# Optimization experiments

Hardware: AMD Instinct MI355X
Metric: run time of the kernel (lower is better)

Reference implementation:

```python
import jax, jax.numpy as jnp
import numpy as np

B, S, D = 2, 2048, 2048
H, HKV = 16, 4
HD = D // H  # 128
ROPE_BASE = 10000.0


def _rope(t, cos, sin):
    # t: [B, h, S, HD]; torch variant: x1 = even dims, x2 = odd dims,
    # output = concat([x1*cos - x2*sin, x1*sin + x2*cos], axis=-1)
    x1 = t[..., ::2]
    x2 = t[..., 1::2]
    return jnp.concatenate([x1 * cos - x2 * sin, x1 * sin + x2 * cos], axis=-1)


def setup_inputs() -> dict:
    key = jax.random.key(0)
    kx, kq, kk, kv, ko = jax.random.split(key, 5)
    x = jax.random.normal(kx, (B, S, D), dtype=jnp.float32)
    scale = 0.02
    Wq = jax.random.normal(kq, (D, H * HD), dtype=jnp.float32) * scale
    Wk = jax.random.normal(kk, (D, HKV * HD), dtype=jnp.float32) * scale
    Wv = jax.random.normal(kv, (D, HKV * HD), dtype=jnp.float32) * scale
    Wo = jax.random.normal(ko, (H * HD, D), dtype=jnp.float32) * scale
    mask = jnp.tril(jnp.ones((S, S), dtype=bool))  # causal
    return {"x": x, "Wq": Wq, "Wk": Wk, "Wv": Wv, "Wo": Wo, "mask": mask}


def reference(x, Wq, Wk, Wv, Wo, mask):
    b, s, d = x.shape
    # projections: [B,S,h,HD] -> [B,h,S,HD]
    q = (x @ Wq).reshape(b, s, H, HD).transpose(0, 2, 1, 3)
    k = (x @ Wk).reshape(b, s, HKV, HD).transpose(0, 2, 1, 3)
    v = (x @ Wv).reshape(b, s, HKV, HD).transpose(0, 2, 1, 3)

    # RoPE tables: [S, HD/2]
    theta = 1.0 / (ROPE_BASE ** (jnp.arange(0, HD, 2, dtype=jnp.float32) / HD))
    angles = jnp.arange(s, dtype=jnp.float32)[:, None] * theta
    cos, sin = jnp.cos(angles), jnp.sin(angles)

    q = _rope(q, cos, sin)
    k = _rope(k, cos, sin)

    # GQA: repeat_interleave kv heads along head dim
    rep = H // HKV
    k = jnp.repeat(k, rep, axis=1)
    v = jnp.repeat(v, rep, axis=1)

    scores = jnp.einsum("bhqd,bhkd->bhqk", q, k) / jnp.sqrt(jnp.float32(HD))
    scores = jnp.where(mask, scores, -jnp.inf)
    attn = jax.nn.softmax(scores, axis=-1)

    out = jnp.einsum("bhqk,bhkd->bqhd", attn, v).reshape(b, s, H * HD)
    return out @ Wo
```

## Files before the change

kernel.cpp:

```cpp
#include <hip/hip_runtime.h>

typedef __bf16 bf16;
typedef __bf16 bf16x8 __attribute__((ext_vector_type(8)));
typedef float f32x4 __attribute__((ext_vector_type(4)));
typedef short s16x4 __attribute__((ext_vector_type(4)));

#define B_ 2
#define S_ 2048
#define D_ 2048
#define H_ 16
#define HKV_ 4
#define HD_ 128
#define QKVW 3072
#define QKW 2560
#define SCALE 0.08838834764831845f
#define NEGINF -30000.0f

__device__ inline void gload16(const void* g, void* l) {
  __builtin_amdgcn_global_load_lds((const __attribute__((address_space(1))) unsigned int*)g,
                                   (__attribute__((address_space(3))) unsigned int*)l, 16, 0, 0);
}

__device__ inline unsigned short bfb(float v) {
  union { bf16 h; unsigned short u; } c;
  c.h = (bf16)v;
  return c.u;
}

__global__ void detect_dtype(const unsigned* __restrict__ xw, int* __restrict__ flag) {
  __shared__ int cnt;
  if (threadIdx.x == 0) cnt = 0;
  __syncthreads();
  unsigned w = xw[(size_t)threadIdx.x * 16384];
  unsigned low = w & 0xFFFFu;
  int e = (int)((low >> 7) & 0xFF);
  int vote = (low == 0u || (e >= 100 && e <= 140)) ? 1 : 0;
  atomicAdd(&cnt, vote);
  __syncthreads();
  if (threadIdx.x == 0) *flag = (cnt >= 128) ? 1 : 0;
}

__global__ __launch_bounds__(256) void transpose_qkvw(
    const void* __restrict__ Wq, const void* __restrict__ Wk, const void* __restrict__ Wv,
    bf16* __restrict__ wqkvT, const int* __restrict__ flag) {
  int z = blockIdx.z;
  const void* in = (z == 0) ? Wq : (z == 1) ? Wk : Wv;
  int cols = (z == 0) ? 2048 : 512;
  bf16* out = wqkvT + ((z == 0) ? 0 : (z == 1) ? 2048 * 2048 : 2560 * 2048);
  if (blockIdx.x * 32 >= cols) return;
  int fm = *flag;
  __shared__ float tile[32][33];
  int c0 = blockIdx.x * 32, r0 = blockIdx.y * 32;
  int tx = threadIdx.x, ty = threadIdx.y;
#pragma unroll
  for (int i = 0; i < 32; i += 8) {
    long idx = (long)(r0 + ty + i) * cols + c0 + tx;
    tile[ty + i][tx] = fm ? (float)((const bf16*)in)[idx] : ((const float*)in)[idx];
  }
  __syncthreads();
#pragma unroll
  for (int i = 0; i < 32; i += 8)
    out[(long)(c0 + ty + i) * 2048 + r0 + tx] = (bf16)tile[tx][ty + i];
}

__global__ __launch_bounds__(256) void transpose_cvt(
    const void* __restrict__ in, bf16* __restrict__ out,
    long in_stride, long out_stride, const int* __restrict__ flag) {
  __shared__ float tile[32][33];
  int fm = *flag;
  int c0 = blockIdx.x * 32, r0 = blockIdx.y * 32;
  int tx = threadIdx.x, ty = threadIdx.y;
#pragma unroll
  for (int i = 0; i < 32; i += 8) {
    long idx = (long)(r0 + ty + i) * in_stride + c0 + tx;
    tile[ty + i][tx] = fm ? (float)((const bf16*)in)[idx] : ((const float*)in)[idx];
  }
  __syncthreads();
#pragma unroll
  for (int i = 0; i < 32; i += 8)
    out[(long)(c0 + ty + i) * out_stride + r0 + tx] = (bf16)tile[tx][ty + i];
}

#define BM 128
#define BN 128
#define BK 32

__global__ __launch_bounds__(256) void gemm_bt(
    const void* __restrict__ A, const bf16* __restrict__ Bt, void* __restrict__ C,
    int M, int N, int K, int ldc, int ncmax,
    bf16* __restrict__ vt_out, int vcol0,
    const int* __restrict__ flag, int adyn, int cdyn) {
  alignas(16) __shared__ bf16 la[BM * BK];
  alignas(16) __shared__ bf16 lb[BN * BK];
  int fm = flag ? *flag : 1;
  bool af32 = adyn && !fm;
  bool cf32 = cdyn && !fm;
  int tid = threadIdx.x;
  int wave = tid >> 6, lane = tid & 63;
  int wr = wave >> 1, wc = wave & 1;
  int quad = lane >> 4, l16 = lane & 15;
  int m0 = blockIdx.y * BM, n0 = blockIdx.x * BN;

  f32x4 acc[4][4] = {};

  int sr = (wave << 4) + (lane >> 2);
  int sc = (lane & 3) << 3;
  const bf16* gb0 = Bt + (long)(n0 + sr) * K + sc;
  const bf16* gb1 = Bt + (long)(n0 + 64 + sr) * K + sc;
  bf16* lb0 = lb + (wave << 9);
  bf16* lb1 = lb + 2048 + (wave << 9);
  bf16* la0 = la + (wave << 9);
  bf16* la1 = la + 2048 + (wave << 9);
  const bf16* ga0 = nullptr; const bf16* ga1 = nullptr;
  const float* gaf = nullptr;
  int fr = tid >> 1, fh = (tid & 1) << 4;
  if (af32) gaf = (const float*)A + (long)(m0 + fr) * K + fh;
  else { ga0 = (const bf16*)A + (long)(m0 + sr) * K + sc;
         ga1 = (const bf16*)A + (long)(m0 + 64 + sr) * K + sc; }
  bf16* law = la + fr * BK + fh;

  for (int k0 = 0; k0 < K; k0 += BK) {
    __syncthreads();
    gload16(gb0 + k0, lb0);
    gload16(gb1 + k0, lb1);
    if (af32) {
      const float* fp = gaf + k0;
      alignas(16) bf16 t[16];
#pragma unroll
      for (int u = 0; u < 16; u += 4) {
        float4 f = *(const float4*)(fp + u);
        t[u] = (bf16)f.x; t[u + 1] = (bf16)f.y; t[u + 2] = (bf16)f.z; t[u + 3] = (bf16)f.w;
      }
      *(uint4*)law = *(uint4*)t;
      *(uint4*)(law + 8) = *(uint4*)(t + 8);
    } else {
      gload16(ga0 + k0, la0);
      gload16(ga1 + k0, la1);
    }
    __syncthreads();

    const bf16* pa = la + ((wr << 6) + l16) * BK + (quad << 3);
    const bf16* pb = lb + ((wc << 6) + l16) * BK + (quad << 3);
    bf16x8 af[4], bfr[4];
#pragma unroll
    for (int i = 0; i < 4; i++) af[i] = *(const bf16x8*)(pa + (i << 4) * BK);
#pragma unroll
    for (int j = 0; j < 4; j++) bfr[j] = *(const bf16x8*)(pb + (j << 4) * BK);
#pragma unroll
    for (int i = 0; i < 4; i++)
#pragma unroll
      for (int j = 0; j < 4; j++)
        acc[i][j] = __builtin_amdgcn_mfma_f32_16x16x32_bf16(af[i], bfr[j], acc[i][j], 0, 0, 0);
  }

  if (vt_out && n0 >= vcol0) {
#pragma unroll
    for (int i = 0; i < 4; i++)
#pragma unroll
      for (int j = 0; j < 4; j++) {
        int col = n0 + (wc << 6) + (j << 4) + l16;
        int hdg = col - vcol0;
        int row0 = m0 + (wr << 6) + (i << 4) + (quad << 2);
        int bb = row0 >> 11, s = row0 & 2047;
        ushort4 p;
        p.x = bfb(acc[i][j][0]); p.y = bfb(acc[i][j][1]);
        p.z = bfb(acc[i][j][2]); p.w = bfb(acc[i][j][3]);
        *(ushort4*)(vt_out + (((long)(bb * 512 + hdg)) << 11) + s) = p;
      }
  } else {
#pragma unroll
    for (int i = 0; i < 4; i++)
#pragma unroll
      for (int j = 0; j < 4; j++) {
        int col = n0 + (wc << 6) + (j << 4) + l16;
        if (col >= ncmax) continue;
#pragma unroll
        for (int r = 0; r < 4; r++) {
          long row = m0 + (wr << 6) + (i << 4) + (quad << 2) + r;
          float v = acc[i][j][r];
          if (cf32) ((float*)C)[row * ldc + col] = v;
          else      ((bf16*)C)[row * ldc + col] = (bf16)v;
        }
      }
  }
}

__global__ __launch_bounds__(256) void rope_scatter(
    const bf16* __restrict__ qkv, bf16* __restrict__ Q, bf16* __restrict__ Ko) {
  int row = blockIdx.x;
  int b = row >> 11, s = row & 2047;
  int tid = threadIdx.x;
  const bf16* src = qkv + (long)row * QKW;
#pragma unroll
  for (int it = 0; it < 4; ++it) {
    int p = tid + it * 256;
    int h = p >> 6, i = p & 63;
    float x1 = (float)src[h * 128 + 2 * i];
    float x2 = (float)src[h * 128 + 2 * i + 1];
    float theta = __expf(-0.14391156831212787f * (float)i);
    float sn, cs;
    sincosf((float)s * theta, &sn, &cs);
    long qb = ((long)(b * H_ + h) * S_ + s) * HD_;
    Q[qb + i]      = (bf16)((x1 * cs - x2 * sn) * SCALE);
    Q[qb + 64 + i] = (bf16)((x1 * sn + x2 * cs) * SCALE);
  }
  {
    int kh = tid >> 6, i = tid & 63;
    float x1 = (float)src[2048 + kh * 128 + 2 * i];
    float x2 = (float)src[2048 + kh * 128 + 2 * i + 1];
    float theta = __expf(-0.14391156831212787f * (float)i);
    float sn, cs;
    sincosf((float)s * theta, &sn, &cs);
    long kb = ((long)(b * HKV_ + kh) * S_ + s) * HD_;
    Ko[kb + i]      = (bf16)(x1 * cs - x2 * sn);
    Ko[kb + 64 + i] = (bf16)(x1 * sn + x2 * cs);
  }
}

#define KTILE 8192
#define VTILE 8192

__global__ __launch_bounds__(256) void attn_kernel(
    const bf16* __restrict__ Q, const bf16* __restrict__ K,
    const bf16* __restrict__ Vt, bf16* __restrict__ O) {
  alignas(16) __shared__ bf16 Ks[2 * KTILE];
  alignas(16) __shared__ bf16 Vs[2 * VTILE];
  int qt0 = blockIdx.x;
  int h = blockIdx.y, b = blockIdx.z;
  int kh = h >> 2;
  int tid = threadIdx.x, wave = tid >> 6, lane = tid & 63;
  int quad = lane >> 4, l16 = lane & 15;
  const bf16* Kg = K + ((long)(b * HKV_ + kh) * S_) * HD_;
  const bf16* Vg = Vt + ((long)(b * HKV_ + kh) * HD_) * S_;

  int kgo[4], vgo[4], klo[4], vlo[4];
#pragma unroll
  for (int u = 0; u < 4; u++) {
    int i = u * 4 + wave;
    int r = i * 4 + quad;
    int c = l16 ^ (r & 15);
    kgo[u] = r * HD_ + c * 8;
    klo[u] = i * 512;
    int v = i * 8 + (lane >> 3);
    int cv = (lane & 7) ^ (v & 7);
    vgo[u] = v * S_ + cv * 8;
    vlo[u] = i * 512;
  }

  for (int hf = 0; hf < 2; ++hf) {
    int qt = hf ? 31 - qt0 : qt0;
    int q0 = qt * 64;
    const bf16* Qg = Q + ((long)(b * H_ + h) * S_ + q0) * HD_;

    bf16x8 qb[4];
    {
      const bf16* qrow = Qg + (wave * 16 + l16) * HD_ + quad * 8;
#pragma unroll
      for (int kk = 0; kk < 4; kk++) qb[kk] = *(const bf16x8*)(qrow + kk * 32);
    }

    if (hf) __syncthreads();

#pragma unroll
    for (int u = 0; u < 4; u++) {
      gload16(Kg + kgo[u], Ks + klo[u]);
      gload16(Vg + vgo[u], Vs + vlo[u]);
    }

    f32x4 Of[8] = {};
    float m_run = NEGINF, l_run = 0.f;

    for (int kt = 0; kt <= qt; ++kt) {
      __syncthreads();
      int p = kt & 1;
      if (kt < qt) {
        const bf16* kn = Kg + (long)(kt + 1) * 8192;
        const bf16* vn = Vg + (long)(kt + 1) * 64;
        bf16* kd = Ks + (p ^ 1) * KTILE;
        bf16* vd = Vs + (p ^ 1) * VTILE;
#pragma unroll
        for (int u = 0; u < 4; u++) {
          gload16(kn + kgo[u], kd + klo[u]);
          gload16(vn + vgo[u], vd + vlo[u]);
        }
      }
      const bf16* kc = Ks + p * KTILE;
      const bf16* vc = Vs + p * VTILE;

      bool diag = (kt == qt);
      f32x4 sf[4];
      __builtin_amdgcn_s_setprio(1);
#pragma unroll
      for (int jb = 0; jb < 4; jb++) {
        if (diag && jb > wave) {
          sf[jb] = (f32x4){NEGINF, NEGINF, NEGINF, NEGINF};
        } else {
          f32x4 a = {};
          const bf16* kbase = kc + (jb * 16 + l16) * 128;
#pragma unroll
          for (int kk = 0; kk < 4; kk++) {
            bf16x8 kf = *(const bf16x8*)(kbase + (((kk * 4 + quad) ^ l16) * 8));
            a = __builtin_amdgcn_mfma_f32_16x16x32_bf16(kf, qb[kk], a, 0, 0, 0);
          }
          sf[jb] = a;
        }
      }
      __builtin_amdgcn_s_setprio(0);
      if (diag) {
#pragma unroll
        for (int jb = 0; jb < 4; jb++)
          if (jb == wave) {
#pragma unroll
            for (int r = 0; r < 4; r++)
              if (quad * 4 + r > l16) sf[jb][r] = NEGINF;
          }
      }

      float mx = NEGINF;
#pragma unroll
      for (int jb = 0; jb < 4; jb++)
#pragma unroll
        for (int r = 0; r < 4; r++) mx = fmaxf(mx, sf[jb][r]);
      mx = fmaxf(mx, __shfl_xor(mx, 16));
      mx = fmaxf(mx, __shfl_xor(mx, 32));
      if (__any(mx > m_run + 8.0f)) {
        float mnew = fmaxf(m_run, mx);
        float alpha = __expf(m_run - mnew);
        m_run = mnew;
        l_run *= alpha;
#pragma unroll
        for (int n = 0; n < 8; n++) Of[n] *= alpha;
      }

      float ls = 0.f;
      s16x4 pk[4];
#pragma unroll
      for (int jb = 0; jb < 4; jb++) {
        float p0 = __expf(sf[jb][0] - m_run);
        float p1 = __expf(sf[jb][1] - m_run);
        float p2 = __expf(sf[jb][2] - m_run);
        float p3 = __expf(sf[jb][3] - m_run);
        ls += (p0 + p1) + (p2 + p3);
        s16x4 t;
        t.x = (short)bfb(p0); t.y = (short)bfb(p1);
        t.z = (short)bfb(p2); t.w = (short)bfb(p3);
        pk[jb] = t;
      }
      l_run += ls;

      __builtin_amdgcn_s_setprio(1);
#pragma unroll
      for (int jb = 0; jb < 4; jb++) {
        if (diag && jb > wave) continue;
#pragma unroll
        for (int n = 0; n < 8; n++) {
          int v = n * 16 + l16;
          const bf16* va_p = vc + v * 64 + (((jb * 2 + (quad >> 1)) ^ (l16 & 7)) * 8) + (quad & 1) * 4;
          s16x4 va = *(const s16x4*)va_p;
          Of[n] = __builtin_amdgcn_mfma_f32_16x16x16bf16_1k(va, pk[jb], Of[n], 0, 0, 0);
        }
      }
      __builtin_amdgcn_s_setprio(0);
    }

    l_run += __shfl_xor(l_run, 16);
    l_run += __shfl_xor(l_run, 32);
    float inv = 1.0f / fmaxf(l_run, 1e-30f);
    bf16* Ob = O + ((long)(b * S_) + q0 + wave * 16 + l16) * D_ + h * HD_;
#pragma unroll
    for (int n = 0; n < 8; n++) {
      ushort4 w;
      w.x = bfb(Of[n][0] * inv); w.y = bfb(Of[n][1] * inv);
      w.z = bfb(Of[n][2] * inv); w.w = bfb(Of[n][3] * inv);
      *(ushort4*)(Ob + n * 16 + quad * 4) = w;
    }
  }
}

extern "C" void kernel_launch(void* const* d_in, const int* in_sizes, int n_in,
                              void* d_out, int out_size, void* d_ws, size_t ws_size,
                              hipStream_t stream) {
  const void* x  = d_in[0];
  const void* Wq = d_in[1];
  const void* Wk = d_in[2];
  const void* Wv = d_in[3];
  const void* Wo = d_in[4];
  bf16* ws = (bf16*)d_ws;
  int* flag = (int*)d_ws;

  bf16* qkv   = ws + 16;
  bf16* Vtb   = ws + 10485776;
  bf16* Qb    = ws + 12582928;
  bf16* wqkvT = ws + 12582928;
  bf16* Kb    = ws + 20971536;
  bf16* attno = ws + 16;
  bf16* woT   = ws + 10485776;

  dim3 tb(32, 8);
  detect_dtype<<<1, 256, 0, stream>>>((const unsigned*)x, flag);
  transpose_qkvw<<<dim3(64, 64, 3), tb, 0, stream>>>(Wq, Wk, Wv, wqkvT, flag);
  gemm_bt<<<dim3(QKVW / BN, (B_ * S_) / BM), 256, 0, stream>>>(
      x, wqkvT, qkv, B_ * S_, QKVW, D_, QKW, QKW, Vtb, QKW, flag, 1, 0);
  rope_scatter<<<B_ * S_, 256, 0, stream>>>(qkv, Qb, Kb);
  attn_kernel<<<dim3(S_ / 128, H_, B_), 256, 0, stream>>>(Qb, Kb, Vtb, attno);
  transpose_cvt<<<dim3(64, 64, 1), tb, 0, stream>>>(Wo, woT, 2048, 2048, flag);
  gemm_bt<<<dim3(D_ / BN, (B_ * S_) / BM), 256, 0, stream>>>(
      attno, woT, d_out, B_ * S_, D_, D_, D_, D_, nullptr, 0, flag, 0, 1);
}
```

Measured before the change: 401.7 us.

## Double-buffer GEMM LDS tiles and remap workgroups across XCDs

The GEMM kernel now keeps two LDS buffers for A and B and prefetches the next K tile while running MFMAs on the current one, which drops one barrier per iteration and overlaps global loads with compute. For f32 A inputs the next tile is loaded into registers early and converted and stored to LDS after the MFMAs. Workgroup indices are also remapped so that consecutive tiles go to the same XCD (8-way interleave), aiming for better L2 reuse. The cost is double the LDS use, which may lower occupancy, and the remap assumes the workgroup count is divisible by 8.

```diff
diff --git a/kernel.cpp b/kernel.cpp
--- a/kernel.cpp
+++ b/kernel.cpp
@@ -90,8 +90,8 @@
     int M, int N, int K, int ldc, int ncmax,
     bf16* __restrict__ vt_out, int vcol0,
     const int* __restrict__ flag, int adyn, int cdyn) {
-  alignas(16) __shared__ bf16 la[BM * BK];
-  alignas(16) __shared__ bf16 lb[BN * BK];
+  alignas(16) __shared__ bf16 la[2 * BM * BK];
+  alignas(16) __shared__ bf16 lb[2 * BN * BK];
   int fm = flag ? *flag : 1;
   bool af32 = adyn && !fm;
   bool cf32 = cdyn && !fm;
@@ -99,7 +99,13 @@
   int wave = tid >> 6, lane = tid & 63;
   int wr = wave >> 1, wc = wave & 1;
   int quad = lane >> 4, l16 = lane & 15;
-  int m0 = blockIdx.y * BM, n0 = blockIdx.x * BN;
+
+  int nwg = (int)(gridDim.x * gridDim.y);
+  int flat = (int)(blockIdx.y * gridDim.x + blockIdx.x);
+  int cpx = nwg >> 3;
+  int wk = (flat & 7) * cpx + (flat >> 3);
+  int bx = wk % (int)gridDim.x, by = wk / (int)gridDim.x;
+  int m0 = by * BM, n0 = bx * BN;
 
   f32x4 acc[4][4] = {};
 
@@ -107,40 +113,60 @@
   int sc = (lane & 3) << 3;
   const bf16* gb0 = Bt + (long)(n0 + sr) * K + sc;
   const bf16* gb1 = Bt + (long)(n0 + 64 + sr) * K + sc;
-  bf16* lb0 = lb + (wave << 9);
-  bf16* lb1 = lb + 2048 + (wave << 9);
-  bf16* la0 = la + (wave << 9);
-  bf16* la1 = la + 2048 + (wave << 9);
+  int lo0 = (wave << 9);
+  int lo1 = 2048 + (wave << 9);
   const bf16* ga0 = nullptr; const bf16* ga1 = nullptr;
   const float* gaf = nullptr;
   int fr = tid >> 1, fh = (tid & 1) << 4;
   if (af32) gaf = (const float*)A + (long)(m0 + fr) * K + fh;
   else { ga0 = (const bf16*)A + (long)(m0 + sr) * K + sc;
          ga1 = (const bf16*)A + (long)(m0 + 64 + sr) * K + sc; }
-  bf16* law = la + fr * BK + fh;
-
-  for (int k0 = 0; k0 < K; k0 += BK) {
-    __syncthreads();
-    gload16(gb0 + k0, lb0);
-    gload16(gb1 + k0, lb1);
-    if (af32) {
-      const float* fp = gaf + k0;
-      alignas(16) bf16 t[16];
-#pragma unroll
-      for (int u = 0; u < 16; u += 4) {
-        float4 f = *(const float4*)(fp + u);
-        t[u] = (bf16)f.x; t[u + 1] = (bf16)f.y; t[u + 2] = (bf16)f.z; t[u + 3] = (bf16)f.w;
-      }
-      *(uint4*)law = *(uint4*)t;
-      *(uint4*)(law + 8) = *(uint4*)(t + 8);
-    } else {
-      gload16(ga0 + k0, la0);
-      gload16(ga1 + k0, la1);
-    }
-    __syncthreads();
-
-    const bf16* pa = la + ((wr << 6) + l16) * BK + (quad << 3);
-    const bf16* pb = lb + ((wc << 6) + l16) * BK + (quad << 3);
+  int lawo = fr * BK + fh;
+
+  int nk = K / BK;
+
+  gload16(gb0, lb + lo0);
+  gload16(gb1, lb + lo1);
+  if (af32) {
+    float4 f0[4];
+#pragma unroll
+    for (int u = 0; u < 4; u++) f0[u] = *(const float4*)(gaf + 4 * u);
+    alignas(16) bf16 tt[16];
+#pragma unroll
+    for (int u = 0; u < 4; u++) {
+      tt[4 * u] = (bf16)f0[u].x; tt[4 * u + 1] = (bf16)f0[u].y;
+      tt[4 * u + 2] = (bf16)f0[u].z; tt[4 * u + 3] = (bf16)f0[u].w;
+    }
+    *(uint4*)(la + lawo) = *(uint4*)tt;
+    *(uint4*)(la + lawo + 8) = *(uint4*)(tt + 8);
+  } else {
+    gload16(ga0, la + lo0);
+    gload16(ga1, la + lo1);
+  }
+  __syncthreads();
+
+  for (int t = 0; t < nk; ++t) {
+    int cur = t & 1, nxt = cur ^ 1;
+    const bf16* laC = la + (cur << 12);
+    const bf16* lbC = lb + (cur << 12);
+    bool hasnext = (t + 1 < nk);
+    float4 f[4];
+    if (hasnext) {
+      int k0 = (t + 1) * BK;
+      gload16(gb0 + k0, lb + (nxt << 12) + lo0);
+      gload16(gb1 + k0, lb + (nxt << 12) + lo1);
+      if (af32) {
+        const float* fp = gaf + k0;
+#pragma unroll
+        for (int u = 0; u < 4; u++) f[u] = *(const float4*)(fp + 4 * u);
+      } else {
+        gload16(ga0 + k0, la + (nxt << 12) + lo0);
+        gload16(ga1 + k0, la + (nxt << 12) + lo1);
+      }
+    }
+
+    const bf16* pa = laC + ((wr << 6) + l16) * BK + (quad << 3);
+    const bf16* pb = lbC + ((wc << 6) + l16) * BK + (quad << 3);
     bf16x8 af[4], bfr[4];
 #pragma unroll
     for (int i = 0; i < 4; i++) af[i] = *(const bf16x8*)(pa + (i << 4) * BK);
@@ -151,6 +177,18 @@
 #pragma unroll
       for (int j = 0; j < 4; j++)
         acc[i][j] = __builtin_amdgcn_mfma_f32_16x16x32_bf16(af[i], bfr[j], acc[i][j], 0, 0, 0);
+
+    if (hasnext && af32) {
+      alignas(16) bf16 tt[16];
+#pragma unroll
+      for (int u = 0; u < 4; u++) {
+        tt[4 * u] = (bf16)f[u].x; tt[4 * u + 1] = (bf16)f[u].y;
+        tt[4 * u + 2] = (bf16)f[u].z; tt[4 * u + 3] = (bf16)f[u].w;
+      }
+      *(uint4*)(la + (nxt << 12) + lawo) = *(uint4*)tt;
+      *(uint4*)(la + (nxt << 12) + lawo + 8) = *(uint4*)(tt + 8);
+    }
+    __syncthreads();
   }
 
   if (vt_out && n0 >= vcol0) {
```

Measured after the change: 383.3 us. 4.6% less time.
